# Performance work log

Measured on AMD Instinct MI355X. Metric: run time of the kernel, lower is better.

Reference implementation:

```python
import jax, jax.numpy as jnp
import numpy as np

CLIP_FRAMES = 16
CLIP_STRIDE = 8
D_CODE = 256
K_CODE = 8192
ENC_DIM = 128 * CLIP_FRAMES * 4 * 4  # 32768
EPS = 1e-5


def setup_inputs() -> dict:
    key = jax.random.key(0)
    ks = jax.random.split(key, 16)
    rn = lambda k, s, sc: (jax.random.normal(k, s, jnp.float32) * sc)
    inp = {}
    inp['x'] = jax.random.normal(ks[0], (4, 3, 64, 96, 96), jnp.float32)
    inp['conv1_w'] = rn(ks[1], (32, 3, 3, 3, 3), 0.1)
    inp['conv1_b'] = jnp.zeros((32,), jnp.float32)
    inp['bn1_g'] = jnp.ones((32,), jnp.float32)
    inp['bn1_b'] = jnp.zeros((32,), jnp.float32)
    inp['conv2_w'] = rn(ks[2], (64, 32, 3, 3, 3), 0.05)
    inp['conv2_b'] = jnp.zeros((64,), jnp.float32)
    inp['bn2_g'] = jnp.ones((64,), jnp.float32)
    inp['bn2_b'] = jnp.zeros((64,), jnp.float32)
    inp['conv3_w'] = rn(ks[3], (128, 64, 3, 3, 3), 0.04)
    inp['conv3_b'] = jnp.zeros((128,), jnp.float32)
    inp['bn3_g'] = jnp.ones((128,), jnp.float32)
    inp['bn3_b'] = jnp.zeros((128,), jnp.float32)
    inp['proj_w'] = rn(ks[4], (D_CODE, ENC_DIM), 0.005)
    inp['proj_b'] = jnp.zeros((D_CODE,), jnp.float32)
    inp['codebook'] = jax.random.uniform(ks[5], (K_CODE, D_CODE), jnp.float32, -1.0 / K_CODE, 1.0 / K_CODE)
    inp['gru_w_ih'] = rn(ks[6], (3 * D_CODE, D_CODE), 0.05)
    inp['gru_w_hh'] = rn(ks[7], (3 * D_CODE, D_CODE), 0.05)
    inp['gru_b_ih'] = jnp.zeros((3 * D_CODE,), jnp.float32)
    inp['gru_b_hh'] = jnp.zeros((3 * D_CODE,), jnp.float32)
    return inp


def _conv3d(x, w, b):
    y = jax.lax.conv_general_dilated(x, w, (1, 1, 1), ((1, 1), (1, 1), (1, 1)),
                                     dimension_numbers=('NCDHW', 'OIDHW', 'NCDHW'))
    return y + b[None, :, None, None, None]


def _bn(x, g, b):
    # training-mode BatchNorm3d: batch stats over (N,D,H,W), biased variance
    m = x.mean(axis=(0, 2, 3, 4), keepdims=True)
    v = ((x - m) ** 2).mean(axis=(0, 2, 3, 4), keepdims=True)
    return g[None, :, None, None, None] * (x - m) * jax.lax.rsqrt(v + EPS) + b[None, :, None, None, None]


def _maxpool(x):
    return jax.lax.reduce_window(x, -jnp.inf, jax.lax.max, (1, 1, 1, 2, 2), (1, 1, 1, 2, 2), 'VALID')


def _adaptive_avgpool(x):
    # [N,128,16,24,24] -> [N,128,16,4,4]; 24/4=6 exact window
    s = jax.lax.reduce_window(x, 0.0, jax.lax.add, (1, 1, 1, 6, 6), (1, 1, 1, 6, 6), 'VALID')
    return s / 36.0


def _gru(xs, w_ih, w_hh, b_ih, b_hh):
    # torch GRU, batch_first, h0=0. xs: [B,L,D]
    B, L, D = xs.shape
    gx = jnp.einsum('bld,gd->blg', xs, w_ih) + b_ih  # [B,L,3D]

    def step(h, gx_t):
        gh = h @ w_hh.T + b_hh
        xr, xz, xn = jnp.split(gx_t, 3, axis=-1)
        hr, hz, hn = jnp.split(gh, 3, axis=-1)
        r = jax.nn.sigmoid(xr + hr)
        z = jax.nn.sigmoid(xz + hz)
        n = jnp.tanh(xn + r * hn)
        h2 = (1.0 - z) * n + z * h
        return h2, h2

    h0 = jnp.zeros((B, D), xs.dtype)
    _, ys = jax.lax.scan(step, h0, jnp.swapaxes(gx, 0, 1))
    return jnp.swapaxes(ys, 0, 1)  # [B,L,D]


def _forward(x, conv1_w, conv1_b, bn1_g, bn1_b, conv2_w, conv2_b, bn2_g, bn2_b,
             conv3_w, conv3_b, bn3_g, bn3_b, proj_w, proj_b, codebook,
             gru_w_ih, gru_w_hh, gru_b_ih, gru_b_hh):
    B, C, T, H, W = x.shape
    num_clips = max(1, (T - CLIP_FRAMES) // CLIP_STRIDE + 1)
    clips = jnp.stack([x[:, :, i * CLIP_STRIDE:i * CLIP_STRIDE + CLIP_FRAMES] for i in range(num_clips)])

    def encode(clip):  # clip: [B,3,16,96,96]; BN stats per-clip like the torch loop
        h = jax.nn.relu(_bn(_conv3d(clip, conv1_w, conv1_b), bn1_g, bn1_b))
        h = _maxpool(h)
        h = jax.nn.relu(_bn(_conv3d(h, conv2_w, conv2_b), bn2_g, bn2_b))
        h = _maxpool(h)
        h = jax.nn.relu(_bn(_conv3d(h, conv3_w, conv3_b), bn3_g, bn3_b))
        h = _adaptive_avgpool(h)            # [B,128,16,4,4]
        h = h.reshape(B, -1)                # [B, 32768]
        return h @ proj_w.T + proj_b        # [B, D_CODE]

    features = jnp.swapaxes(jax.vmap(encode)(clips), 0, 1)  # [B,L,D]
    L, D = features.shape[1], features.shape[2]

    # quantize: squared-Euclidean argmin (same argmin as torch.cdist p=2)
    flat = features.reshape(-1, D)
    d2 = (flat * flat).sum(-1, keepdims=True) - 2.0 * flat @ codebook.T + (codebook * codebook).sum(-1)
    token_indices = jnp.argmin(d2, axis=-1)
    quantized = codebook[token_indices].reshape(B, L, D)

    sg = jax.lax.stop_gradient
    commitment_loss = jnp.mean((features - sg(quantized)) ** 2)
    codebook_loss = jnp.mean((quantized - sg(features)) ** 2)
    context_features = _gru(quantized[:, :-1], gru_w_ih, gru_w_hh, gru_b_ih, gru_b_hh)
    context_loss = jnp.mean((context_features - features[:, 1:]) ** 2)
    vq_loss = commitment_loss + 0.25 * codebook_loss + 0.1 * context_loss
    return token_indices.reshape(B, L), quantized, commitment_loss, codebook_loss, context_loss, vq_loss


def reference(x, conv1_w, conv1_b, bn1_g, bn1_b, conv2_w, conv2_b, bn2_g, bn2_b,
              conv3_w, conv3_b, bn3_g, bn3_b, proj_w, proj_b, codebook,
              gru_w_ih, gru_w_hh, gru_b_ih, gru_b_hh):
    return _forward(x, conv1_w, conv1_b, bn1_g, bn1_b, conv2_w, conv2_b, bn2_g, bn2_b,
                    conv3_w, conv3_b, bn3_g, bn3_b, proj_w, proj_b, codebook,
                    gru_w_ih, gru_w_hh, gru_b_ih, gru_b_hh)
```

## Files before the change

### kernel.cpp

```cpp
#include <hip/hip_runtime.h>
#include <math.h>


typedef __attribute__((ext_vector_type(8))) short short8;
typedef __attribute__((ext_vector_type(4))) float f32x4;

__device__ inline unsigned short f2bf(float x) {
    unsigned int u = __float_as_uint(x);
    u += 0x7FFFu + ((u >> 16) & 1u);
    return (unsigned short)(u >> 16);
}
__device__ inline float bf2f(unsigned short h) {
    return __uint_as_float(((unsigned int)h) << 16);
}
__device__ inline f32x4 vmax4(f32x4 a, f32x4 b) {
    return (f32x4){fmaxf(a.x, b.x), fmaxf(a.y, b.y), fmaxf(a.z, b.z), fmaxf(a.w, b.w)};
}
__device__ inline f32x4 vmin4(f32x4 a, f32x4 b) {
    return (f32x4){fminf(a.x, b.x), fminf(a.y, b.y), fminf(a.z, b.z), fminf(a.w, b.w)};
}

#define MF(d, a, b) d = __builtin_amdgcn_mfma_f32_16x16x32_bf16(a, b, d, 0, 0, 0)

#define C1LOADR(J) \
    f32x4 u = *(const f32x4*)(ip + (J) * 36); \
    f32x4 w4 = *(const f32x4*)(ip + (J) * 36 + 4); \
    f32x4 sA = u; \
    f32x4 sB = __builtin_shufflevector(u, w4, 1, 2, 3, 4); \
    f32x4 sC = __builtin_shufflevector(u, w4, 2, 3, 4, 5);
#define C1UPD0(I) a0_##I += wa0 * sA + wa1 * sB + wa2 * sC; a1_##I += wb0 * sA + wb1 * sB + wb2 * sC;
#define C1UPD1(I) a0_##I += wa3 * sA + wa4 * sB + wa5 * sC; a1_##I += wb3 * sA + wb4 * sB + wb5 * sC;
#define C1UPD2(I) a0_##I += wa6 * sA + wa7 * sB + wa8 * sC; a1_##I += wb6 * sA + wb7 * sB + wb8 * sC;

__launch_bounds__(256, 3)
__global__ void conv1k(const float* __restrict__ x, const float* __restrict__ wgt,
                       const float* __restrict__ bias, float* __restrict__ pmax,
                       float* __restrict__ pmin, float* __restrict__ stats, int t0) {
    int bb = blockIdx.x;
    int xt = bb % 3; int yt = (bb / 3) % 4; int t = (bb / 12) % 16; int n = bb / 192;
    int x0 = xt * 32, y0 = yt * 24;
    __shared__ float tile[9 * 936];
    __shared__ float wl[3456];
    __shared__ float sst[64];
    int tid = threadIdx.x;
    for (int i = tid; i < 3456; i += 256) {
        int idx = i % 12; int r = i / 12;
        int co = r & 31; int p = r >> 5;
        wl[i] = idx < 9 ? wgt[co * 81 + p * 9 + idx] : 0.f;
    }
    if (tid < 64) sst[tid] = 0.f;
    for (int i = tid; i < 7956; i += 256) {
        int p = i / 884; int rem = i % 884;
        int r = rem / 34, cl = rem % 34;
        int ci = p / 3, kt = p % 3;
        int lt = t + kt - 1;
        int yy = y0 + r - 1, xx = x0 + cl - 1;
        float v = 0.f;
        if (lt >= 0 && lt <= 15 && yy >= 0 && yy < 96 && xx >= 0 && xx < 96)
            v = x[((size_t)(n * 3 + ci) * 64 + (t0 + lt)) * 9216 + yy * 96 + cl + x0 - 1];
        tile[p * 936 + r * 36 + cl] = v;
    }
    __syncthreads();

    int cg = tid & 15;
    int co0 = cg * 2;
    float bv0 = bias[co0], bv1 = bias[co0 + 1];
    float ls0 = 0.f, lq0 = 0.f, ls1 = 0.f, lq1 = 0.f;
    size_t nt48 = (size_t)(n * 16 + t) * 48;

    #pragma unroll 1
    for (int rr = 0; rr < 3; ++rr) {
        int sp = rr * 16 + (tid >> 4);
        int tx = sp & 7, ty = sp >> 3;
        f32x4 a0_0 = (f32x4)bv0, a0_1 = (f32x4)bv0, a0_2 = (f32x4)bv0, a0_3 = (f32x4)bv0;
        f32x4 a1_0 = (f32x4)bv1, a1_1 = (f32x4)bv1, a1_2 = (f32x4)bv1, a1_3 = (f32x4)bv1;

        #pragma unroll 1
        for (int p = 0; p < 9; ++p) {
            const float* wpk = wl + ((p * 32 + co0) * 12);
            f32x4 wv0 = *(const f32x4*)(wpk);
            f32x4 wv1 = *(const f32x4*)(wpk + 4);
            f32x4 wv2 = *(const f32x4*)(wpk + 8);
            f32x4 wv3 = *(const f32x4*)(wpk + 12);
            f32x4 wv4 = *(const f32x4*)(wpk + 16);
            f32x4 wv5 = *(const f32x4*)(wpk + 20);
            float wa0 = wv0.x, wa1 = wv0.y, wa2 = wv0.z, wa3 = wv0.w;
            float wa4 = wv1.x, wa5 = wv1.y, wa6 = wv1.z, wa7 = wv1.w;
            float wa8 = wv2.x;
            float wb0 = wv3.x, wb1 = wv3.y, wb2 = wv3.z, wb3 = wv3.w;
            float wb4 = wv4.x, wb5 = wv4.y, wb6 = wv4.z, wb7 = wv4.w;
            float wb8 = wv5.x;
            const float* ip = tile + p * 936 + (ty * 4) * 36 + tx * 4;
            { C1LOADR(0) C1UPD0(0) }
            { C1LOADR(1) C1UPD0(1) C1UPD1(0) }
            { C1LOADR(2) C1UPD0(2) C1UPD1(1) C1UPD2(0) }
            { C1LOADR(3) C1UPD0(3) C1UPD1(2) C1UPD2(1) }
            { C1LOADR(4) C1UPD1(3) C1UPD2(2) }
            { C1LOADR(5) C1UPD2(3) }
        }

        f32x4 s4 = a0_0 + a0_1 + a0_2 + a0_3;
        ls0 += s4.x + s4.y + s4.z + s4.w;
        f32x4 q4 = a0_0 * a0_0 + a0_1 * a0_1 + a0_2 * a0_2 + a0_3 * a0_3;
        lq0 += q4.x + q4.y + q4.z + q4.w;
        f32x4 s5 = a1_0 + a1_1 + a1_2 + a1_3;
        ls1 += s5.x + s5.y + s5.z + s5.w;
        f32x4 q5 = a1_0 * a1_0 + a1_1 * a1_1 + a1_2 * a1_2 + a1_3 * a1_3;
        lq1 += q5.x + q5.y + q5.z + q5.w;

        f32x4 mx0a = vmax4(a0_0, a0_1), mx0b = vmax4(a0_2, a0_3);
        f32x4 mn0a = vmin4(a0_0, a0_1), mn0b = vmin4(a0_2, a0_3);
        f32x4 mx1a = vmax4(a1_0, a1_1), mx1b = vmax4(a1_2, a1_3);
        f32x4 mn1a = vmin4(a1_0, a1_1), mn1b = vmin4(a1_2, a1_3);
        size_t row0 = (nt48 + (size_t)(yt * 12 + ty * 2)) * 1536 + (size_t)(xt * 16 + tx * 2) * 32 + co0;
        size_t row1 = row0 + 1536;
        *(float2*)(pmax + row0)      = make_float2(fmaxf(mx0a.x, mx0a.y), fmaxf(mx1a.x, mx1a.y));
        *(float2*)(pmax + row0 + 32) = make_float2(fmaxf(mx0a.z, mx0a.w), fmaxf(mx1a.z, mx1a.w));
        *(float2*)(pmax + row1)      = make_float2(fmaxf(mx0b.x, mx0b.y), fmaxf(mx1b.x, mx1b.y));
        *(float2*)(pmax + row1 + 32) = make_float2(fmaxf(mx0b.z, mx0b.w), fmaxf(mx1b.z, mx1b.w));
        *(float2*)(pmin + row0)      = make_float2(fminf(mn0a.x, mn0a.y), fminf(mn1a.x, mn1a.y));
        *(float2*)(pmin + row0 + 32) = make_float2(fminf(mn0a.z, mn0a.w), fminf(mn1a.z, mn1a.w));
        *(float2*)(pmin + row1)      = make_float2(fminf(mn0b.x, mn0b.y), fminf(mn1b.x, mn1b.y));
        *(float2*)(pmin + row1 + 32) = make_float2(fminf(mn0b.z, mn0b.w), fminf(mn1b.z, mn1b.w));
    }

    ls0 += __shfl_xor(ls0, 16, 64); ls0 += __shfl_xor(ls0, 32, 64);
    lq0 += __shfl_xor(lq0, 16, 64); lq0 += __shfl_xor(lq0, 32, 64);
    ls1 += __shfl_xor(ls1, 16, 64); ls1 += __shfl_xor(ls1, 32, 64);
    lq1 += __shfl_xor(lq1, 16, 64); lq1 += __shfl_xor(lq1, 32, 64);
    if ((tid & 63) < 16) {
        atomicAdd(&sst[co0 * 2], ls0);
        atomicAdd(&sst[co0 * 2 + 1], lq0);
        atomicAdd(&sst[co0 * 2 + 2], ls1);
        atomicAdd(&sst[co0 * 2 + 3], lq1);
    }
    __syncthreads();
    if (tid < 64) atomicAdd(&stats[tid], sst[tid]);
}

__global__ void bnpool1b(const float* __restrict__ pmax, const float* __restrict__ pmin,
                         const float* __restrict__ st, const float* __restrict__ gam,
                         const float* __restrict__ bet,
                         unsigned short* __restrict__ phi, unsigned short* __restrict__ plo) {
    int i = blockIdx.x * 256 + threadIdx.x;
    int c8 = i & 3; int xo = (i >> 2) % 48; int yo = (i / 192) % 48;
    int t = (i / 9216) % 16; int n = i / 147456;
    size_t base = (((size_t)(n * 16 + t) * 48 + yo) * 48 + xo) * 32 + c8 * 8;
    union { unsigned short s[8]; uint4 v; } Uh, Ul;
    #pragma unroll
    for (int j = 0; j < 8; ++j) {
        int ch = c8 * 8 + j;
        float mean = st[ch * 2] * (1.f / 589824.f);
        float var  = st[ch * 2 + 1] * (1.f / 589824.f) - mean * mean;
        var = var < 0.f ? 0.f : var;
        float sc = gam[ch] / sqrtf(var + 1e-5f);
        float sh = bet[ch] - mean * sc;
        float pv = sc >= 0.f ? pmax[base + j] : pmin[base + j];
        float v = fmaxf(sc * pv + sh, 0.f);
        Uh.s[j] = f2bf(v);
        Ul.s[j] = f2bf(v - bf2f(Uh.s[j]));
    }
    size_t off = ((((size_t)n * 18 + t + 1) * 50 + yo + 1) * 52 + (xo + 1)) * 32 + c8 * 8;
    *(uint4*)(phi + off) = Uh.v;
    *(uint4*)(plo + off) = Ul.v;
}

__launch_bounds__(256, 3)
__global__ void conv2k(const unsigned short* __restrict__ phi, const unsigned short* __restrict__ plo,
                       const unsigned short* __restrict__ w2p, const float* __restrict__ bias,
                       float* __restrict__ out, float* __restrict__ st) {
    __shared__ unsigned short tin[12 * 52 * 40];
    float (*sred)[64] = (float (*)[64])(tin);
    float (*qred)[64] = (float (*)[64])(tin + 512);
    int b = blockIdx.x;
    int k8 = b & 7, i96 = b >> 3;
    int n = k8 >> 1, th = k8 & 1;
    int tt = i96 / 12; int y0 = (i96 - tt * 12) * 4;
    int t = th * 8 + tt;
    int wv = threadIdx.x >> 6, lane = threadIdx.x & 63;
    int c = lane & 15, q = lane >> 4;
    int y = y0 + wv;

    f32x4 acc[4][3];
    #pragma unroll
    for (int i = 0; i < 4; ++i)
        #pragma unroll
        for (int j = 0; j < 3; ++j) acc[i][j] = (f32x4)0.f;

    const int loff = c * 32 + q * 8;
    const unsigned short* tb0 = tin + (wv * 52 + c) * 40 + q * 8;
    const unsigned short* tb1 = tb0 + 16 * 40;
    const unsigned short* tb2 = tb0 + 32 * 40;

    #pragma unroll 1
    for (int kt = 0; kt < 3; ++kt) {
        const unsigned short* srch = phi + (size_t)(n * 18 + t + kt) * (50 * 52 * 32);
        const unsigned short* srcl = plo + (size_t)(n * 18 + t + kt) * (50 * 52 * 32);
        const unsigned short* wkt = w2p + kt * 36864;
        __syncthreads();
        for (int i = threadIdx.x; i < 2496; i += 256) {
            int g = i & 3; int xx = (i >> 2) % 52; int rh = (i >> 2) / 52;
            int row = rh % 6; int h = rh / 6;
            const unsigned short* src = (h ? srcl : srch) + (size_t)(y0 + row) * 1664 + xx * 32 + g * 8;
            *(uint4*)(tin + (rh * 52 + xx) * 40 + (g << 3)) = *(const uint4*)src;
        }
        __syncthreads();
        #pragma unroll
        for (int ky = 0; ky < 3; ++ky) {
            #pragma unroll
            for (int kx = 0; kx < 3; ++kx) {
                const unsigned short* wb = wkt + (ky * 3 + kx) * 4096;
                short8 ah[4], al[4], bh[3], bl[3];
                #pragma unroll
                for (int mb = 0; mb < 4; ++mb) {
                    ah[mb] = *(const short8*)(wb + loff + mb * 512);
                    al[mb] = *(const short8*)(wb + 2048 + loff + mb * 512);
                }
                int off = (ky * 52 + kx) * 40;
                bh[0] = *(const short8*)(tb0 + off);
                bl[0] = *(const short8*)(tb0 + off + 12480);
                bh[1] = *(const short8*)(tb1 + off);
                bl[1] = *(const short8*)(tb1 + off + 12480);
                bh[2] = *(const short8*)(tb2 + off);
                bl[2] = *(const short8*)(tb2 + off + 12480);
                #pragma unroll
                for (int mb = 0; mb < 4; ++mb)
                    #pragma unroll
                    for (int xt = 0; xt < 3; ++xt) {
                        MF(acc[mb][xt], ah[mb], bh[xt]);
                        MF(acc[mb][xt], ah[mb], bl[xt]);
                        MF(acc[mb][xt], al[mb], bh[xt]);
                    }
            }
        }
    }
    __syncthreads();
    float* ob = out + (((size_t)(n * 16 + t) * 48) + y) * (48 * 64);
    #pragma unroll
    for (int mb = 0; mb < 4; ++mb) {
        f32x4 bv = *(const f32x4*)(bias + mb * 16 + q * 4);
        f32x4 v0 = acc[mb][0] + bv, v1 = acc[mb][1] + bv, v2 = acc[mb][2] + bv;
        *(f32x4*)(ob + (0 * 16 + c) * 64 + mb * 16 + q * 4) = v0;
        *(f32x4*)(ob + (1 * 16 + c) * 64 + mb * 16 + q * 4) = v1;
        *(f32x4*)(ob + (2 * 16 + c) * 64 + mb * 16 + q * 4) = v2;
        #pragma unroll
        for (int r = 0; r < 4; ++r) {
            float s  = v0[r] + v1[r] + v2[r];
            float q2 = v0[r] * v0[r] + v1[r] * v1[r] + v2[r] * v2[r];
            #pragma unroll
            for (int m = 1; m < 16; m <<= 1) { s += __shfl_xor(s, m, 64); q2 += __shfl_xor(q2, m, 64); }
            if (c == 0) { sred[wv][mb * 16 + q * 4 + r] = s; qred[wv][mb * 16 + q * 4 + r] = q2; }
        }
    }
    __syncthreads();
    if (threadIdx.x < 64) {
        float s = sred[0][threadIdx.x] + sred[1][threadIdx.x] + sred[2][threadIdx.x] + sred[3][threadIdx.x];
        float q2 = qred[0][threadIdx.x] + qred[1][threadIdx.x] + qred[2][threadIdx.x] + qred[3][threadIdx.x];
        atomicAdd(&st[threadIdx.x * 2], s);
        atomicAdd(&st[threadIdx.x * 2 + 1], q2);
    }
}

__global__ void bnpool2k(const float* __restrict__ cin, const float* __restrict__ st,
                         const float* __restrict__ gam, const float* __restrict__ bet,
                         unsigned short* __restrict__ phi, unsigned short* __restrict__ plo) {
    int i = blockIdx.x * 256 + threadIdx.x;
    if (i >= 509184) return;
    int oc = i & 7; int xp = (i >> 3) % 34; int yp = (i / 272) % 26;
    int tp = (i / 7072) % 18; int n = i / 127296;
    union { unsigned short s[8]; uint4 v; } Uh, Ul;
    if (tp >= 1 && tp <= 16 && yp >= 1 && yp <= 24 && xp >= 1 && xp <= 24) {
        int t = tp - 1, yo = yp - 1, xo = xp - 1;
        const float* b0 = cin + ((((size_t)(n * 16 + t) * 48) + 2 * yo) * 48 + 2 * xo) * 64 + oc * 8;
        #pragma unroll
        for (int j = 0; j < 8; ++j) {
            int ch = oc * 8 + j;
            float mean = st[ch * 2] * (1.f / 147456.f);
            float var  = st[ch * 2 + 1] * (1.f / 147456.f) - mean * mean;
            var = var < 0.f ? 0.f : var;
            float sc = gam[ch] / sqrtf(var + 1e-5f);
            float sh = bet[ch] - mean * sc;
            float a  = b0[j] * sc + sh;
            float bb = b0[64 + j] * sc + sh;
            float c2 = b0[3072 + j] * sc + sh;
            float d  = b0[3136 + j] * sc + sh;
            float v = fmaxf(fmaxf(fmaxf(a, bb), fmaxf(c2, d)), 0.f);
            Uh.s[j] = f2bf(v);
            Ul.s[j] = f2bf(v - bf2f(Uh.s[j]));
        }
    } else {
        Uh.v = make_uint4(0, 0, 0, 0);
        Ul.v = make_uint4(0, 0, 0, 0);
    }
    size_t off = ((((size_t)n * 18 + tp) * 26 + yp) * 34 + xp) * 64 + oc * 8;
    *(uint4*)(phi + off) = Uh.v;
    *(uint4*)(plo + off) = Ul.v;
}

__launch_bounds__(256, 3)
__global__ void conv3k(const unsigned short* __restrict__ phi, const unsigned short* __restrict__ plo,
                       const unsigned short* __restrict__ w3p, const float* __restrict__ bias,
                       float* __restrict__ out, float* __restrict__ st) {
    __shared__ unsigned short tin[12 * 26 * 72];
    float (*sred)[64] = (float (*)[64])(tin);
    float (*qred)[64] = (float (*)[64])(tin + 512);
    int b = blockIdx.x;
    int k8 = b & 7, i96 = b >> 3;
    int n = k8 >> 1, th = k8 & 1;
    int cg = i96 / 48; int r48 = i96 - cg * 48;
    int tt = r48 / 6;  int y0 = (r48 - tt * 6) * 4;
    int t = th * 8 + tt;
    int wv = threadIdx.x >> 6, lane = threadIdx.x & 63;
    int c = lane & 15, q = lane >> 4;
    int y = y0 + wv;

    f32x4 acc[4][2];
    #pragma unroll
    for (int i = 0; i < 4; ++i) { acc[i][0] = (f32x4)0.f; acc[i][1] = (f32x4)0.f; }

    const int loff = c * 32 + q * 8;
    const unsigned short* wkt0 = w3p + (size_t)cg * 221184;
    const unsigned short* vb0 = tin + (wv * 26 + c) * 72 + q * 8;
    int x10 = 16 + 0 + c; x10 = x10 > 25 ? 25 : x10;
    int x11 = 16 + 1 + c; x11 = x11 > 25 ? 25 : x11;
    int x12 = 16 + 2 + c; x12 = x12 > 25 ? 25 : x12;
    const unsigned short* vb1_0 = tin + (wv * 26 + x10) * 72 + q * 8;
    const unsigned short* vb1_1 = tin + (wv * 26 + x11) * 72 + q * 8;
    const unsigned short* vb1_2 = tin + (wv * 26 + x12) * 72 + q * 8;

    #pragma unroll 1
    for (int kt = 0; kt < 3; ++kt) {
        const unsigned short* srch = phi + (size_t)(n * 18 + t + kt) * (26 * 34 * 64);
        const unsigned short* srcl = plo + (size_t)(n * 18 + t + kt) * (26 * 34 * 64);
        const unsigned short* wkt = wkt0 + kt * 73728;
        __syncthreads();
        for (int i = threadIdx.x; i < 2496; i += 256) {
            int g = i & 7; int xx = (i >> 3) % 26; int rh = (i >> 3) / 26;
            int row = rh % 6; int h = rh / 6;
            const unsigned short* src = (h ? srcl : srch) + (size_t)(y0 + row) * 2176 + xx * 64 + g * 8;
            *(uint4*)(tin + (rh * 26 + xx) * 72 + (g << 3)) = *(const uint4*)src;
        }
        __syncthreads();
        #pragma unroll
        for (int ky = 0; ky < 3; ++ky) {
            #pragma unroll
            for (int kx = 0; kx < 3; ++kx) {
                #pragma unroll
                for (int kc = 0; kc < 2; ++kc) {
                    const unsigned short* wb = wkt + ky * 24576 + kx * 8192 + kc * 2048;
                    short8 ah[4], al[4], bh[2], bl[2];
                    #pragma unroll
                    for (int mb = 0; mb < 4; ++mb) {
                        ah[mb] = *(const short8*)(wb + loff + mb * 512);
                        al[mb] = *(const short8*)(wb + 4096 + loff + mb * 512);
                    }
                    int off0 = ky * 1872 + kx * 72 + kc * 32;
                    int off1 = ky * 1872 + kc * 32;
                    const unsigned short* vb1 = (kx == 0) ? vb1_0 : (kx == 1) ? vb1_1 : vb1_2;
                    bh[0] = *(const short8*)(vb0 + off0);
                    bl[0] = *(const short8*)(vb0 + off0 + 11232);
                    bh[1] = *(const short8*)(vb1 + off1);
                    bl[1] = *(const short8*)(vb1 + off1 + 11232);
                    #pragma unroll
                    for (int mb = 0; mb < 4; ++mb)
                        #pragma unroll
                        for (int xt = 0; xt < 2; ++xt) {
                            MF(acc[mb][xt], ah[mb], bh[xt]);
                            MF(acc[mb][xt], ah[mb], bl[xt]);
                            MF(acc[mb][xt], al[mb], bh[xt]);
                        }
                }
            }
        }
    }
    __syncthreads();
    float* ob = out + (((size_t)(n * 16 + t) * 24) + y) * (24 * 128) + cg * 64;
    #pragma unroll
    for (int mb = 0; mb < 4; ++mb) {
        f32x4 bv = *(const f32x4*)(bias + cg * 64 + mb * 16 + q * 4);
        f32x4 v0 = acc[mb][0] + bv;
        f32x4 v1 = acc[mb][1] + bv;
        *(f32x4*)(ob + c * 128 + mb * 16 + q * 4) = v0;
        if (c < 8) *(f32x4*)(ob + (16 + c) * 128 + mb * 16 + q * 4) = v1;
        #pragma unroll
        for (int r = 0; r < 4; ++r) {
            float s  = v0[r] + (c < 8 ? v1[r] : 0.f);
            float q2 = v0[r] * v0[r] + (c < 8 ? v1[r] * v1[r] : 0.f);
            #pragma unroll
            for (int m = 1; m < 16; m <<= 1) { s += __shfl_xor(s, m, 64); q2 += __shfl_xor(q2, m, 64); }
            if (c == 0) { sred[wv][mb * 16 + q * 4 + r] = s; qred[wv][mb * 16 + q * 4 + r] = q2; }
        }
    }
    __syncthreads();
    if (threadIdx.x < 64) {
        int co = cg * 64 + threadIdx.x;
        float s = sred[0][threadIdx.x] + sred[1][threadIdx.x] + sred[2][threadIdx.x] + sred[3][threadIdx.x];
        float q2 = qred[0][threadIdx.x] + qred[1][threadIdx.x] + qred[2][threadIdx.x] + qred[3][threadIdx.x];
        atomicAdd(&st[co * 2], s);
        atomicAdd(&st[co * 2 + 1], q2);
    }
}

__global__ void bnavgk(const float* __restrict__ x, const float* __restrict__ st,
                       const float* __restrict__ gam, const float* __restrict__ bet,
                       float* __restrict__ enc) {
    int i = blockIdx.x * 256 + threadIdx.x;
    int c = i & 127; int xo = (i >> 7) & 3; int yo = (i >> 9) & 3;
    int t = (i >> 11) & 15; int n = i >> 15;
    float mean = st[c * 2] * (1.f / 36864.f);
    float var  = st[c * 2 + 1] * (1.f / 36864.f) - mean * mean;
    var = var < 0.f ? 0.f : var;
    float sc = gam[c] / sqrtf(var + 1e-5f);
    float sh = bet[c] - mean * sc;
    const float* base = x + ((((size_t)(n * 16 + t) * 24) + yo * 6) * 24 + xo * 6) * 128 + c;
    float s = 0.f;
    #pragma unroll
    for (int wy = 0; wy < 6; ++wy)
        #pragma unroll
        for (int wx = 0; wx < 6; ++wx)
            s += fmaxf(base[(wy * 24 + wx) * 128] * sc + sh, 0.f);
    enc[(size_t)n * 32768 + (size_t)c * 256 + t * 16 + yo * 4 + xo] = s * (1.f / 36.f);
}

__global__ void prep2k(const float* __restrict__ c2w, unsigned short* __restrict__ w2p) {
    int i = blockIdx.x * 256 + threadIdx.x;
    if (i >= 110592) return;
    int ci = i & 31; int co = (i >> 5) & 63; int h = (i >> 11) & 1;
    int o = (i >> 12) % 9; int kt = i / 36864;
    int ky = o / 3, kx = o % 3;
    float w = c2w[(((size_t)(co * 32 + ci) * 3 + kt) * 3 + ky) * 3 + kx];
    unsigned short hi = f2bf(w);
    w2p[i] = h ? f2bf(w - bf2f(hi)) : hi;
}
__global__ void prep3k(const float* __restrict__ c3w, unsigned short* __restrict__ w3p) {
    int i = blockIdx.x * 256 + threadIdx.x;
    if (i >= 442368) return;
    int cil = i & 31; int cop = (i >> 5) & 63; int kc = (i >> 11) & 1; int h = (i >> 12) & 1;
    int kx = (i >> 13) % 3; int ky = (i / 24576) % 3; int kt = (i / 73728) % 3; int cg = i / 221184;
    int ci = kc * 32 + cil; int co = cg * 64 + cop;
    float w = c3w[(((size_t)(co * 64 + ci) * 3 + kt) * 3 + ky) * 3 + kx];
    unsigned short hi = f2bf(w);
    w3p[i] = h ? f2bf(w - bf2f(hi)) : hi;
}
__global__ void prepwhhk(const float* __restrict__ whh, float* __restrict__ wt) {
    int i = blockIdx.x * 256 + threadIdx.x;
    int g = i % 768, k = i / 768;
    wt[i] = whh[(size_t)g * 256 + k];
}

__global__ void transck(const float* __restrict__ cb, float* __restrict__ cbT) {
    __shared__ float t[32][33];
    int bx = blockIdx.x & 255;
    int by = blockIdx.x >> 8;
    int ld = threadIdx.x & 31, lk = threadIdx.x >> 5;
    #pragma unroll
    for (int i = 0; i < 4; ++i) {
        int kl = lk + i * 8;
        t[kl][ld] = cb[(size_t)(bx * 32 + kl) * 256 + by * 32 + ld];
    }
    __syncthreads();
    #pragma unroll
    for (int i = 0; i < 4; ++i) {
        int dl = lk + i * 8;
        cbT[(size_t)(by * 32 + dl) * 8192 + bx * 32 + ld] = t[ld][dl];
    }
}

__global__ void cnormk(const float* __restrict__ cbT, double* __restrict__ cn2) {
    int k = blockIdx.x * 256 + threadIdx.x;
    double s = 0.0;
    for (int d = 0; d < 256; ++d) {
        double c = (double)cbT[(size_t)d * 8192 + k];
        s += c * c;
    }
    cn2[k] = s;
}

__global__ void projinitk(const float* __restrict__ pb, float* __restrict__ feat) {
    int i = blockIdx.x * 256 + threadIdx.x;
    feat[i] = pb[i & 255];
}

__global__ void projk(const float* __restrict__ enc, const float* __restrict__ pw,
                      float* __restrict__ feat) {
    int d = blockIdx.x & 255; int ch = blockIdx.x >> 8;
    int k0 = ch * 4096;
    float acc[28];
    #pragma unroll
    for (int e = 0; e < 28; ++e) acc[e] = 0.f;
    const float* wrow = pw + (size_t)d * 32768 + k0;
    for (int k = threadIdx.x; k < 4096; k += 256) {
        float wv = wrow[k];
        #pragma unroll
        for (int e = 0; e < 28; ++e) acc[e] += enc[(size_t)e * 32768 + k0 + k] * wv;
    }
    __shared__ float red[4 * 28];
    #pragma unroll
    for (int e = 0; e < 28; ++e) {
        float v = acc[e];
        #pragma unroll
        for (int o = 32; o > 0; o >>= 1) v += __shfl_down(v, o, 64);
        if ((threadIdx.x & 63) == 0) red[(threadIdx.x >> 6) * 28 + e] = v;
    }
    __syncthreads();
    if (threadIdx.x < 28) {
        int e = threadIdx.x;
        int l = e >> 2, n = e & 3;
        float s = red[e] + red[28 + e] + red[56 + e] + red[84 + e];
        atomicAdd(&feat[(size_t)(n * 7 + l) * 256 + d], s);
    }
}

__global__ void quantk(const float* __restrict__ feat, const float* __restrict__ cbT,
                       const double* __restrict__ cn2, unsigned long long* __restrict__ best) {
    int kc = blockIdx.x & 31, r = blockIdx.x >> 5;
    int k = kc * 256 + threadIdx.x;
    __shared__ float fs[256];
    fs[threadIdx.x] = feat[(size_t)r * 256 + threadIdx.x];
    __syncthreads();
    double dot = 0.0;
    for (int d = 0; d < 256; ++d)
        dot += (double)cbT[(size_t)d * 8192 + k] * (double)fs[d];
    float s = (float)(cn2[k] - 2.0 * dot);
    unsigned int bits = __float_as_uint(s);
    unsigned int key = (bits & 0x80000000u) ? ~bits : (bits | 0x80000000u);
    unsigned long long p = ((unsigned long long)key << 32) | (unsigned int)k;
    #pragma unroll
    for (int o = 32; o > 0; o >>= 1) {
        unsigned long long qv = __shfl_down(p, o, 64);
        if (qv < p) p = qv;
    }
    if ((threadIdx.x & 63) == 0) atomicMin(&best[r], p);
}

__global__ void gatherk(const unsigned long long* __restrict__ best,
                        const float* __restrict__ feat, const float* __restrict__ cb,
                        float* __restrict__ dout, float* __restrict__ quant,
                        float* __restrict__ acc) {
    int r = blockIdx.x;
    int d = threadIdx.x;
    int idx = (int)(best[r] & 0xFFFFFFFFull);
    float q = cb[(size_t)idx * 256 + d];
    quant[r * 256 + d] = q;
    dout[28 + r * 256 + d] = q;
    if (d == 0) dout[r] = (float)idx;
    float df = feat[r * 256 + d] - q;
    float v = df * df;
    #pragma unroll
    for (int o = 32; o > 0; o >>= 1) v += __shfl_down(v, o, 64);
    if ((d & 63) == 0) atomicAdd(&acc[0], v);
}

__global__ void gxk(const float* __restrict__ quant, const float* __restrict__ wih,
                    const float* __restrict__ bih, float* __restrict__ gx) {
    int o = blockIdx.x * 256 + threadIdx.x;
    int g = o % 768; int t = (o / 768) % 6; int n = o / (768 * 6);
    const float* q = quant + (size_t)(n * 7 + t) * 256;
    const float* w = wih + (size_t)g * 256;
    float s = bih[g];
    #pragma unroll 4
    for (int d = 0; d < 256; ++d) s += q[d] * w[d];
    gx[o] = s;
}

__global__ void gru_allk(const float* __restrict__ gx, const float* __restrict__ wt,
                         const float* __restrict__ bhh, const float* __restrict__ feat,
                         float* __restrict__ acc) {
    int b = blockIdx.x;
    int d = threadIdx.x;
    __shared__ float hs[256];
    hs[d] = 0.f;
    __syncthreads();
    float ctx = 0.f;
    for (int t = 0; t < 6; ++t) {
        float g0 = bhh[d], g1 = bhh[256 + d], g2 = bhh[512 + d];
        #pragma unroll 4
        for (int k = 0; k < 256; ++k) {
            float hv = hs[k];
            const float* wr = wt + (size_t)k * 768;
            g0 += wr[d] * hv; g1 += wr[256 + d] * hv; g2 += wr[512 + d] * hv;
        }
        const float* gxr = gx + (size_t)(b * 6 + t) * 768;
        float xr = gxr[d], xz = gxr[256 + d], xn = gxr[512 + d];
        float rr = 1.f / (1.f + expf(-(xr + g0)));
        float zz = 1.f / (1.f + expf(-(xz + g1)));
        float nn = tanhf(xn + rr * g2);
        float h2 = (1.f - zz) * nn + zz * hs[d];
        __syncthreads();
        hs[d] = h2;
        __syncthreads();
        float df = h2 - feat[(size_t)(b * 7 + t + 1) * 256 + d];
        ctx += df * df;
    }
    #pragma unroll
    for (int o = 32; o > 0; o >>= 1) ctx += __shfl_down(ctx, o, 64);
    if ((d & 63) == 0) atomicAdd(&acc[1], ctx);
}

__global__ void fink(const float* __restrict__ acc, float* __restrict__ dout) {
    float comm = acc[0] / 7168.f;
    float ctx  = acc[1] / 6144.f;
    dout[7196] = comm;
    dout[7197] = comm;
    dout[7198] = ctx;
    dout[7199] = comm + 0.25f * comm + 0.1f * ctx;
}

extern "C" void kernel_launch(void* const* d_in, const int* in_sizes, int n_in,
                              void* d_out, int out_size, void* d_ws, size_t ws_size,
                              hipStream_t stream) {
    (void)in_sizes; (void)n_in; (void)out_size; (void)ws_size;
    const float* x    = (const float*)d_in[0];
    const float* c1w  = (const float*)d_in[1];
    const float* c1b  = (const float*)d_in[2];
    const float* bn1g = (const float*)d_in[3];
    const float* bn1b = (const float*)d_in[4];
    const float* c2w  = (const float*)d_in[5];
    const float* c2b  = (const float*)d_in[6];
    const float* bn2g = (const float*)d_in[7];
    const float* bn2b = (const float*)d_in[8];
    const float* c3w  = (const float*)d_in[9];
    const float* c3b  = (const float*)d_in[10];
    const float* bn3g = (const float*)d_in[11];
    const float* bn3b = (const float*)d_in[12];
    const float* pw   = (const float*)d_in[13];
    const float* pb   = (const float*)d_in[14];
    const float* cb   = (const float*)d_in[15];
    const float* wih  = (const float*)d_in[16];
    const float* whh  = (const float*)d_in[17];
    const float* bih  = (const float*)d_in[18];
    const float* bhh  = (const float*)d_in[19];
    float* out = (float*)d_out;

    char* w = (char*)d_ws;
    float* A  = (float*)w;                         w += 75497472;
    float* PMAX = A;
    float* PMIN = A + 4718592;
    float* cbT = A;
    double* cn2 = (double*)((char*)A + 8388608);
    char*  SH = w;                                 w += 16293888;
    unsigned short* P3h = (unsigned short*)SH;
    unsigned short* P3l = (unsigned short*)(SH + 8146944);
    unsigned short* P2h = (unsigned short*)w;      w += 11980800;
    unsigned short* P2l = (unsigned short*)w;      w += 11980800;
    unsigned short* W2P = (unsigned short*)w;      w += 221184;
    unsigned short* W3P = (unsigned short*)w;      w += 884736;
    float* WT    = (float*)w;                      w += 786432;
    float* enc   = (float*)w;                      w += 3670016;
    float* feat  = (float*)w;                      w += 28672;
    float* quant = (float*)w;                      w += 28672;
    float* gx    = (float*)w;                      w += 73728;
    float* statsA = (float*)w;                     w += 21504;
    float* acc    = (float*)w;                     w += 16;
    unsigned long long* best = (unsigned long long*)w;  w += 224;

    hipMemsetAsync(P2h, 0, 11980800 * 2, stream);
    hipMemsetAsync(statsA, 0, 21504 + 16, stream);
    hipMemsetAsync(best, 0xFF, 224, stream);
    prep2k<<<432, 256, 0, stream>>>(c2w, W2P);
    prep3k<<<1728, 256, 0, stream>>>(c3w, W3P);
    prepwhhk<<<768, 256, 0, stream>>>(whh, WT);

    for (int l = 0; l < 7; ++l) {
        float* st1 = statsA + (l * 3 + 0) * 256;
        float* st2 = statsA + (l * 3 + 1) * 256;
        float* st3 = statsA + (l * 3 + 2) * 256;
        conv1k<<<768, 256, 0, stream>>>(x, c1w, c1b, PMAX, PMIN, st1, l * 8);
        bnpool1b<<<2304, 256, 0, stream>>>(PMAX, PMIN, st1, bn1g, bn1b, P2h, P2l);
        conv2k<<<768, 256, 0, stream>>>(P2h, P2l, W2P, c2b, A, st2);
        bnpool2k<<<1989, 256, 0, stream>>>(A, st2, bn2g, bn2b, P3h, P3l);
        conv3k<<<768, 256, 0, stream>>>(P3h, P3l, W3P, c3b, A, st3);
        bnavgk<<<512, 256, 0, stream>>>(A, st3, bn3g, bn3b, enc + (size_t)l * 131072);
    }

    transck<<<2048, 256, 0, stream>>>(cb, cbT);
    cnormk<<<32, 256, 0, stream>>>(cbT, cn2);
    projinitk<<<28, 256, 0, stream>>>(pb, feat);
    projk<<<2048, 256, 0, stream>>>(enc, pw, feat);
    quantk<<<896, 256, 0, stream>>>(feat, cbT, cn2, best);
    gatherk<<<28, 256, 0, stream>>>(best, feat, cb, out, quant, acc);
    gxk<<<72, 256, 0, stream>>>(quant, wih, bih, gx);
    gru_allk<<<4, 256, 0, stream>>>(gx, WT, bhh, feat, acc);
    fink<<<1, 1, 0, stream>>>(acc, out);
}
```

Before: 2.323 ms.

## Retile conv2/conv3 warps to 2x2 row-channel blocks, swizzle conv3 LDS, vectorize projection

In conv2k and conv3k each wave now covers two output rows and half of the output channels, instead of one row and all channels. This halves the per-wave weight (A-operand) global loads and raises reuse of the loaded weights across rows. conv3k drops the padded LDS row stride of 72 in favour of an XOR swizzle on a 64-wide layout to avoid bank conflicts. projk is rewritten so each block handles 8 output dims with float4 loads and warp-level reduction, launching 256 blocks instead of 2048, which changes parallelism and atomic count.

```diff
diff --git a/kernel.cpp b/kernel.cpp
--- a/kernel.cpp
+++ b/kernel.cpp
@@ -170,27 +170,32 @@
                        const unsigned short* __restrict__ w2p, const float* __restrict__ bias,
                        float* __restrict__ out, float* __restrict__ st) {
     __shared__ unsigned short tin[12 * 52 * 40];
-    float (*sred)[64] = (float (*)[64])(tin);
-    float (*qred)[64] = (float (*)[64])(tin + 512);
+    float (*sred)[32] = (float (*)[32])(tin);
+    float (*qred)[32] = (float (*)[32])(tin + 256);
     int b = blockIdx.x;
     int k8 = b & 7, i96 = b >> 3;
     int n = k8 >> 1, th = k8 & 1;
     int tt = i96 / 12; int y0 = (i96 - tt * 12) * 4;
     int t = th * 8 + tt;
-    int wv = threadIdx.x >> 6, lane = threadIdx.x & 63;
+    int w = threadIdx.x >> 6, lane = threadIdx.x & 63;
     int c = lane & 15, q = lane >> 4;
-    int y = y0 + wv;
-
-    f32x4 acc[4][3];
-    #pragma unroll
-    for (int i = 0; i < 4; ++i)
-        #pragma unroll
-        for (int j = 0; j < 3; ++j) acc[i][j] = (f32x4)0.f;
-
-    const int loff = c * 32 + q * 8;
-    const unsigned short* tb0 = tin + (wv * 52 + c) * 40 + q * 8;
-    const unsigned short* tb1 = tb0 + 16 * 40;
-    const unsigned short* tb2 = tb0 + 32 * 40;
+    int lrow = (w & 1) * 2, h2 = w >> 1;
+
+    f32x4 acc[2][2][3];
+    #pragma unroll
+    for (int i = 0; i < 2; ++i)
+        #pragma unroll
+        for (int j = 0; j < 2; ++j)
+            #pragma unroll
+            for (int k = 0; k < 3; ++k) acc[i][j][k] = (f32x4)0.f;
+
+    const int loff = h2 * 1024 + c * 32 + q * 8;
+    int tbo[2][3];
+    #pragma unroll
+    for (int rr = 0; rr < 2; ++rr)
+        #pragma unroll
+        for (int xt = 0; xt < 3; ++xt)
+            tbo[rr][xt] = ((lrow + rr) * 52 + xt * 16 + c) * 40 + q * 8;
 
     #pragma unroll 1
     for (int kt = 0; kt < 3; ++kt) {
@@ -209,53 +214,62 @@
         for (int ky = 0; ky < 3; ++ky) {
             #pragma unroll
             for (int kx = 0; kx < 3; ++kx) {
-                const unsigned short* wb = wkt + (ky * 3 + kx) * 4096;
-                short8 ah[4], al[4], bh[3], bl[3];
+                const unsigned short* wb = wkt + (ky * 3 + kx) * 4096 + loff;
+                short8 a0 = *(const short8*)(wb);
+                short8 a1 = *(const short8*)(wb + 512);
+                short8 l0 = *(const short8*)(wb + 2048);
+                short8 l1 = *(const short8*)(wb + 2560);
+                int off = (ky * 52 + kx) * 40;
                 #pragma unroll
-                for (int mb = 0; mb < 4; ++mb) {
-                    ah[mb] = *(const short8*)(wb + loff + mb * 512);
-                    al[mb] = *(const short8*)(wb + 2048 + loff + mb * 512);
+                for (int rr = 0; rr < 2; ++rr) {
+                    short8 bh0 = *(const short8*)(tin + tbo[rr][0] + off);
+                    short8 bl0 = *(const short8*)(tin + tbo[rr][0] + off + 12480);
+                    short8 bh1 = *(const short8*)(tin + tbo[rr][1] + off);
+                    short8 bl1 = *(const short8*)(tin + tbo[rr][1] + off + 12480);
+                    short8 bh2 = *(const short8*)(tin + tbo[rr][2] + off);
+                    short8 bl2 = *(const short8*)(tin + tbo[rr][2] + off + 12480);
+                    MF(acc[rr][0][0], a0, bh0); MF(acc[rr][0][0], a0, bl0); MF(acc[rr][0][0], l0, bh0);
+                    MF(acc[rr][0][1], a0, bh1); MF(acc[rr][0][1], a0, bl1); MF(acc[rr][0][1], l0, bh1);
+                    MF(acc[rr][0][2], a0, bh2); MF(acc[rr][0][2], a0, bl2); MF(acc[rr][0][2], l0, bh2);
+                    MF(acc[rr][1][0], a1, bh0); MF(acc[rr][1][0], a1, bl0); MF(acc[rr][1][0], l1, bh0);
+                    MF(acc[rr][1][1], a1, bh1); MF(acc[rr][1][1], a1, bl1); MF(acc[rr][1][1], l1, bh1);
+                    MF(acc[rr][1][2], a1, bh2); MF(acc[rr][1][2], a1, bl2); MF(acc[rr][1][2], l1, bh2);
                 }
-                int off = (ky * 52 + kx) * 40;
-                bh[0] = *(const short8*)(tb0 + off);
-                bl[0] = *(const short8*)(tb0 + off + 12480);
-                bh[1] = *(const short8*)(tb1 + off);
-                bl[1] = *(const short8*)(tb1 + off + 12480);
-                bh[2] = *(const short8*)(tb2 + off);
-                bl[2] = *(const short8*)(tb2 + off + 12480);
-                #pragma unroll
-                for (int mb = 0; mb < 4; ++mb)
-                    #pragma unroll
-                    for (int xt = 0; xt < 3; ++xt) {
-                        MF(acc[mb][xt], ah[mb], bh[xt]);
-                        MF(acc[mb][xt], ah[mb], bl[xt]);
-                        MF(acc[mb][xt], al[mb], bh[xt]);
-                    }
             }
         }
     }
     __syncthreads();
-    float* ob = out + (((size_t)(n * 16 + t) * 48) + y) * (48 * 64);
-    #pragma unroll
-    for (int mb = 0; mb < 4; ++mb) {
-        f32x4 bv = *(const f32x4*)(bias + mb * 16 + q * 4);
-        f32x4 v0 = acc[mb][0] + bv, v1 = acc[mb][1] + bv, v2 = acc[mb][2] + bv;
-        *(f32x4*)(ob + (0 * 16 + c) * 64 + mb * 16 + q * 4) = v0;
-        *(f32x4*)(ob + (1 * 16 + c) * 64 + mb * 16 + q * 4) = v1;
-        *(f32x4*)(ob + (2 * 16 + c) * 64 + mb * 16 + q * 4) = v2;
+    #pragma unroll
+    for (int mbp = 0; mbp < 2; ++mbp) {
+        f32x4 bv = *(const f32x4*)(bias + h2 * 32 + mbp * 16 + q * 4);
+        float s0 = 0.f, s1 = 0.f, s2 = 0.f, s3 = 0.f;
+        float p0 = 0.f, p1 = 0.f, p2 = 0.f, p3 = 0.f;
+        #pragma unroll
+        for (int rr = 0; rr < 2; ++rr) {
+            int y = y0 + lrow + rr;
+            float* ob = out + (((size_t)(n * 16 + t) * 48) + y) * (48 * 64) + h2 * 32 + mbp * 16 + q * 4;
+            #pragma unroll
+            for (int xt = 0; xt < 3; ++xt) {
+                f32x4 v = acc[rr][mbp][xt] + bv;
+                *(f32x4*)(ob + (xt * 16 + c) * 64) = v;
+                s0 += v.x; s1 += v.y; s2 += v.z; s3 += v.w;
+                p0 += v.x * v.x; p1 += v.y * v.y; p2 += v.z * v.z; p3 += v.w * v.w;
+            }
+        }
+        float sv[4] = {s0, s1, s2, s3}, qv[4] = {p0, p1, p2, p3};
         #pragma unroll
         for (int r = 0; r < 4; ++r) {
-            float s  = v0[r] + v1[r] + v2[r];
-            float q2 = v0[r] * v0[r] + v1[r] * v1[r] + v2[r] * v2[r];
+            float s = sv[r], q2 = qv[r];
             #pragma unroll
             for (int m = 1; m < 16; m <<= 1) { s += __shfl_xor(s, m, 64); q2 += __shfl_xor(q2, m, 64); }
-            if (c == 0) { sred[wv][mb * 16 + q * 4 + r] = s; qred[wv][mb * 16 + q * 4 + r] = q2; }
+            if (c == 0) { sred[w][mbp * 16 + q * 4 + r] = s; qred[w][mbp * 16 + q * 4 + r] = q2; }
         }
     }
     __syncthreads();
     if (threadIdx.x < 64) {
-        float s = sred[0][threadIdx.x] + sred[1][threadIdx.x] + sred[2][threadIdx.x] + sred[3][threadIdx.x];
-        float q2 = qred[0][threadIdx.x] + qred[1][threadIdx.x] + qred[2][threadIdx.x] + qred[3][threadIdx.x];
+        int h = threadIdx.x >> 5, loc = threadIdx.x & 31;
+        float s = sred[2 * h][loc] + sred[2 * h + 1][loc];
+        float q2 = qred[2 * h][loc] + qred[2 * h + 1][loc];
         atomicAdd(&st[threadIdx.x * 2], s);
         atomicAdd(&st[threadIdx.x * 2 + 1], q2);
     }
@@ -301,44 +315,38 @@
 __global__ void conv3k(const unsigned short* __restrict__ phi, const unsigned short* __restrict__ plo,
                        const unsigned short* __restrict__ w3p, const float* __restrict__ bias,
                        float* __restrict__ out, float* __restrict__ st) {
-    __shared__ unsigned short tin[12 * 26 * 72];
-    float (*sred)[64] = (float (*)[64])(tin);
-    float (*qred)[64] = (float (*)[64])(tin + 512);
+    __shared__ unsigned short tin[12 * 26 * 64];
+    float (*sred)[32] = (float (*)[32])(tin);
+    float (*qred)[32] = (float (*)[32])(tin + 256);
     int b = blockIdx.x;
     int k8 = b & 7, i96 = b >> 3;
     int n = k8 >> 1, th = k8 & 1;
     int cg = i96 / 48; int r48 = i96 - cg * 48;
     int tt = r48 / 6;  int y0 = (r48 - tt * 6) * 4;
     int t = th * 8 + tt;
-    int wv = threadIdx.x >> 6, lane = threadIdx.x & 63;
+    int w = threadIdx.x >> 6, lane = threadIdx.x & 63;
     int c = lane & 15, q = lane >> 4;
-    int y = y0 + wv;
-
-    f32x4 acc[4][2];
-    #pragma unroll
-    for (int i = 0; i < 4; ++i) { acc[i][0] = (f32x4)0.f; acc[i][1] = (f32x4)0.f; }
-
-    const int loff = c * 32 + q * 8;
-    const unsigned short* wkt0 = w3p + (size_t)cg * 221184;
-    const unsigned short* vb0 = tin + (wv * 26 + c) * 72 + q * 8;
-    int x10 = 16 + 0 + c; x10 = x10 > 25 ? 25 : x10;
-    int x11 = 16 + 1 + c; x11 = x11 > 25 ? 25 : x11;
-    int x12 = 16 + 2 + c; x12 = x12 > 25 ? 25 : x12;
-    const unsigned short* vb1_0 = tin + (wv * 26 + x10) * 72 + q * 8;
-    const unsigned short* vb1_1 = tin + (wv * 26 + x11) * 72 + q * 8;
-    const unsigned short* vb1_2 = tin + (wv * 26 + x12) * 72 + q * 8;
+    int lrow = (w & 1) * 2, h2 = w >> 1;
+
+    f32x4 acc[2][2][2];
+    #pragma unroll
+    for (int i = 0; i < 2; ++i)
+        #pragma unroll
+        for (int j = 0; j < 2; ++j) { acc[i][j][0] = (f32x4)0.f; acc[i][j][1] = (f32x4)0.f; }
+
+    const unsigned short* wsrc = w3p + (size_t)cg * 221184 + h2 * 1024 + c * 32 + q * 8;
 
     #pragma unroll 1
     for (int kt = 0; kt < 3; ++kt) {
         const unsigned short* srch = phi + (size_t)(n * 18 + t + kt) * (26 * 34 * 64);
         const unsigned short* srcl = plo + (size_t)(n * 18 + t + kt) * (26 * 34 * 64);
-        const unsigned short* wkt = wkt0 + kt * 73728;
+        const unsigned short* wkt = wsrc + kt * 73728;
         __syncthreads();
         for (int i = threadIdx.x; i < 2496; i += 256) {
             int g = i & 7; int xx = (i >> 3) % 26; int rh = (i >> 3) / 26;
             int row = rh % 6; int h = rh / 6;
             const unsigned short* src = (h ? srcl : srch) + (size_t)(y0 + row) * 2176 + xx * 64 + g * 8;
-            *(uint4*)(tin + (rh * 26 + xx) * 72 + (g << 3)) = *(const uint4*)src;
+            *(uint4*)(tin + ((rh * 26 + xx) << 6) + ((g ^ (xx & 7)) << 3)) = *(const uint4*)src;
         }
         __syncthreads();
         #pragma unroll
@@ -348,54 +356,65 @@
                 #pragma unroll
                 for (int kc = 0; kc < 2; ++kc) {
                     const unsigned short* wb = wkt + ky * 24576 + kx * 8192 + kc * 2048;
-                    short8 ah[4], al[4], bh[2], bl[2];
+                    short8 a0 = *(const short8*)(wb);
+                    short8 a1 = *(const short8*)(wb + 512);
+                    short8 l0 = *(const short8*)(wb + 4096);
+                    short8 l1 = *(const short8*)(wb + 4608);
+                    int x0 = kx + c;
+                    int x1t = 16 + kx + c;
+                    int x1 = x1t > 25 ? 25 : x1t;
+                    int so0 = ((kc * 4 + q) ^ (x0 & 7)) << 3;
+                    int so1 = ((kc * 4 + q) ^ (x1 & 7)) << 3;
                     #pragma unroll
-                    for (int mb = 0; mb < 4; ++mb) {
-                        ah[mb] = *(const short8*)(wb + loff + mb * 512);
-                        al[mb] = *(const short8*)(wb + 4096 + loff + mb * 512);
+                    for (int rr = 0; rr < 2; ++rr) {
+                        int row = lrow + rr + ky;
+                        short8 bh0 = *(const short8*)(tin + ((row * 26 + x0) << 6) + so0);
+                        short8 bl0 = *(const short8*)(tin + (((6 + row) * 26 + x0) << 6) + so0);
+                        short8 bh1 = *(const short8*)(tin + ((row * 26 + x1) << 6) + so1);
+                        short8 bl1 = *(const short8*)(tin + (((6 + row) * 26 + x1) << 6) + so1);
+                        MF(acc[rr][0][0], a0, bh0); MF(acc[rr][0][0], a0, bl0); MF(acc[rr][0][0], l0, bh0);
+                        MF(acc[rr][0][1], a0, bh1); MF(acc[rr][0][1], a0, bl1); MF(acc[rr][0][1], l0, bh1);
+                        MF(acc[rr][1][0], a1, bh0); MF(acc[rr][1][0], a1, bl0); MF(acc[rr][1][0], l1, bh0);
+                        MF(acc[rr][1][1], a1, bh1); MF(acc[rr][1][1], a1, bl1); MF(acc[rr][1][1], l1, bh1);
                     }
-                    int off0 = ky * 1872 + kx * 72 + kc * 32;
-                    int off1 = ky * 1872 + kc * 32;
-                    const unsigned short* vb1 = (kx == 0) ? vb1_0 : (kx == 1) ? vb1_1 : vb1_2;
-                    bh[0] = *(const short8*)(vb0 + off0);
-                    bl[0] = *(const short8*)(vb0 + off0 + 11232);
-                    bh[1] = *(const short8*)(vb1 + off1);
-                    bl[1] = *(const short8*)(vb1 + off1 + 11232);
-                    #pragma unroll
-                    for (int mb = 0; mb < 4; ++mb)
-                        #pragma unroll
-                        for (int xt = 0; xt < 2; ++xt) {
-                            MF(acc[mb][xt], ah[mb], bh[xt]);
-                            MF(acc[mb][xt], ah[mb], bl[xt]);
-                            MF(acc[mb][xt], al[mb], bh[xt]);
-                        }
                 }
             }
         }
     }
     __syncthreads();
-    float* ob = out + (((size_t)(n * 16 + t) * 24) + y) * (24 * 128) + cg * 64;
-    #pragma unroll
-    for (int mb = 0; mb < 4; ++mb) {
-        f32x4 bv = *(const f32x4*)(bias + cg * 64 + mb * 16 + q * 4);
-        f32x4 v0 = acc[mb][0] + bv;
-        f32x4 v1 = acc[mb][1] + bv;
-        *(f32x4*)(ob + c * 128 + mb * 16 + q * 4) = v0;
-        if (c < 8) *(f32x4*)(ob + (16 + c) * 128 + mb * 16 + q * 4) = v1;
+    #pragma unroll
+    for (int mbp = 0; mbp < 2; ++mbp) {
+        f32x4 bv = *(const f32x4*)(bias + cg * 64 + h2 * 32 + mbp * 16 + q * 4);
+        float s0 = 0.f, s1 = 0.f, s2 = 0.f, s3 = 0.f;
+        float p0 = 0.f, p1 = 0.f, p2 = 0.f, p3 = 0.f;
+        #pragma unroll
+        for (int rr = 0; rr < 2; ++rr) {
+            int y = y0 + lrow + rr;
+            float* ob = out + (((size_t)(n * 16 + t) * 24) + y) * (24 * 128) + cg * 64 + h2 * 32 + mbp * 16 + q * 4;
+            f32x4 v0 = acc[rr][mbp][0] + bv;
+            f32x4 v1 = acc[rr][mbp][1] + bv;
+            *(f32x4*)(ob + c * 128) = v0;
+            if (c < 8) *(f32x4*)(ob + (16 + c) * 128) = v1;
+            float m = c < 8 ? 1.f : 0.f;
+            s0 += v0.x + m * v1.x; s1 += v0.y + m * v1.y; s2 += v0.z + m * v1.z; s3 += v0.w + m * v1.w;
+            p0 += v0.x * v0.x + m * v1.x * v1.x; p1 += v0.y * v0.y + m * v1.y * v1.y;
+            p2 += v0.z * v0.z + m * v1.z * v1.z; p3 += v0.w * v0.w + m * v1.w * v1.w;
+        }
+        float sv[4] = {s0, s1, s2, s3}, qv[4] = {p0, p1, p2, p3};
         #pragma unroll
         for (int r = 0; r < 4; ++r) {
-            float s  = v0[r] + (c < 8 ? v1[r] : 0.f);
-            float q2 = v0[r] * v0[r] + (c < 8 ? v1[r] * v1[r] : 0.f);
+            float s = sv[r], q2 = qv[r];
             #pragma unroll
             for (int m = 1; m < 16; m <<= 1) { s += __shfl_xor(s, m, 64); q2 += __shfl_xor(q2, m, 64); }
-            if (c == 0) { sred[wv][mb * 16 + q * 4 + r] = s; qred[wv][mb * 16 + q * 4 + r] = q2; }
+            if (c == 0) { sred[w][mbp * 16 + q * 4 + r] = s; qred[w][mbp * 16 + q * 4 + r] = q2; }
         }
     }
     __syncthreads();
     if (threadIdx.x < 64) {
+        int h = threadIdx.x >> 5, loc = threadIdx.x & 31;
         int co = cg * 64 + threadIdx.x;
-        float s = sred[0][threadIdx.x] + sred[1][threadIdx.x] + sred[2][threadIdx.x] + sred[3][threadIdx.x];
-        float q2 = qred[0][threadIdx.x] + qred[1][threadIdx.x] + qred[2][threadIdx.x] + qred[3][threadIdx.x];
+        float s = sred[2 * h][loc] + sred[2 * h + 1][loc];
+        float q2 = qred[2 * h][loc] + qred[2 * h + 1][loc];
         atomicAdd(&st[co * 2], s);
         atomicAdd(&st[co * 2 + 1], q2);
     }
@@ -483,31 +502,31 @@
 
 __global__ void projk(const float* __restrict__ enc, const float* __restrict__ pw,
                       float* __restrict__ feat) {
-    int d = blockIdx.x & 255; int ch = blockIdx.x >> 8;
-    int k0 = ch * 4096;
+    int dg = blockIdx.x >> 3, ch = blockIdx.x & 7;
+    int dl = threadIdx.x >> 5, kk = threadIdx.x & 31;
+    int d = dg * 8 + dl;
+    int k0 = ch * 4096 + kk * 4;
+    const float* wrow = pw + (size_t)d * 32768 + k0;
+    const float* ep = enc + k0;
     float acc[28];
     #pragma unroll
     for (int e = 0; e < 28; ++e) acc[e] = 0.f;
-    const float* wrow = pw + (size_t)d * 32768 + k0;
-    for (int k = threadIdx.x; k < 4096; k += 256) {
-        float wv = wrow[k];
-        #pragma unroll
-        for (int e = 0; e < 28; ++e) acc[e] += enc[(size_t)e * 32768 + k0 + k] * wv;
-    }
-    __shared__ float red[4 * 28];
+    #pragma unroll 1
+    for (int i = 0; i < 32; ++i) {
+        f32x4 wv = *(const f32x4*)(wrow + i * 128);
+        #pragma unroll
+        for (int e = 0; e < 28; ++e) {
+            f32x4 ev = *(const f32x4*)(ep + (size_t)e * 32768 + i * 128);
+            acc[e] += wv.x * ev.x + wv.y * ev.y + wv.z * ev.z + wv.w * ev.w;
+        }
+    }
     #pragma unroll
     for (int e = 0; e < 28; ++e) {
         float v = acc[e];
-        #pragma unroll
-        for (int o = 32; o > 0; o >>= 1) v += __shfl_down(v, o, 64);
-        if ((threadIdx.x & 63) == 0) red[(threadIdx.x >> 6) * 28 + e] = v;
-    }
-    __syncthreads();
-    if (threadIdx.x < 28) {
-        int e = threadIdx.x;
-        int l = e >> 2, n = e & 3;
-        float s = red[e] + red[28 + e] + red[56 + e] + red[84 + e];
-        atomicAdd(&feat[(size_t)(n * 7 + l) * 256 + d], s);
+        v += __shfl_xor(v, 1, 64);  v += __shfl_xor(v, 2, 64);
+        v += __shfl_xor(v, 4, 64);  v += __shfl_xor(v, 8, 64);
+        v += __shfl_xor(v, 16, 64);
+        if (kk == 0) atomicAdd(&feat[(size_t)((e & 3) * 7 + (e >> 2)) * 256 + d], v);
     }
 }
 
@@ -676,7 +695,7 @@
     transck<<<2048, 256, 0, stream>>>(cb, cbT);
     cnormk<<<32, 256, 0, stream>>>(cbT, cn2);
     projinitk<<<28, 256, 0, stream>>>(pb, feat);
-    projk<<<2048, 256, 0, stream>>>(enc, pw, feat);
+    projk<<<256, 256, 0, stream>>>(enc, pw, feat);
     quantk<<<896, 256, 0, stream>>>(feat, cbT, cn2, best);
     gatherk<<<28, 256, 0, stream>>>(best, feat, cb, out, quant, acc);
     gxk<<<72, 256, 0, stream>>>(quant, wih, bih, gx);
```

After: 2.392 ms. 1.03x slower.
